# Kernel tuning notes

Measured on AMD Instinct MI355X. Metric: run time of the kernel, lower is better.

The kernel has to match this reference:

```python
import jax, jax.numpy as jnp
import numpy as np

B, N_IN, N_HID, T = 64, 512, 512, 512


def setup_inputs() -> dict:
    key = jax.random.key(0)
    k1, k2, k3, k4, k5 = jax.random.split(key, 5)
    scale = 1.0 / np.sqrt(N_HID).astype(np.float32)
    return {
        "X": jax.random.normal(k1, (B, N_IN, T), dtype=jnp.float32),
        "Wax": jax.random.normal(k2, (N_IN, N_HID), dtype=jnp.float32) * scale,
        "Waa": jax.random.normal(k3, (N_HID, N_HID), dtype=jnp.float32) * scale,
        "bx": jax.random.normal(k4, (N_HID,), dtype=jnp.float32) * scale,
        "ba": jax.random.normal(k5, (N_HID,), dtype=jnp.float32) * scale,
    }


def reference(X, Wax, Waa, bx, ba):
    # X: [B, n_in, T]. a_{t+1} = tanh(x_t @ Wax + bx + a_t @ Waa + ba)
    # Precompute the input projections for all timesteps in one big GEMM:
    # [T, B, n_hid]
    Xt = jnp.transpose(X, (2, 0, 1))  # [T, B, n_in]
    inp_proj = jnp.einsum('tbi,ih->tbh', Xt, Wax) + bx + ba

    def step(a, u):
        a_next = jnp.tanh(u + a @ Waa)
        return a_next, a_next

    a0 = jnp.zeros((X.shape[0], Waa.shape[0]), dtype=X.dtype)
    _, A = jax.lax.scan(step, a0, inp_proj)
    return A  # [T, B, n_hid] == stacked A[1:] of the torch module
```

## Files before the change

kernel.cpp:

```cpp
#include <hip/hip_runtime.h>
#include <math.h>

#define BB   64
#define NIN  512
#define NH   512
#define TT   512

typedef _Float16 half2_t __attribute__((ext_vector_type(2)));

__device__ __forceinline__ unsigned pk16(float x, float y) {
    unsigned lo = (unsigned)__builtin_bit_cast(unsigned short, (_Float16)x);
    unsigned hi = (unsigned)__builtin_bit_cast(unsigned short, (_Float16)y);
    return lo | (hi << 16);
}

__device__ __forceinline__ float dot2u(unsigned w, unsigned a, float acc) {
    return __builtin_amdgcn_fdot2(__builtin_bit_cast(half2_t, w),
                                  __builtin_bit_cast(half2_t, a), acc, false);
}

__device__ __forceinline__ float tanh_fast(float x) {
    float ax = __builtin_fabsf(x);
    float e  = __builtin_amdgcn_exp2f(-2.885390082f * ax);
    float r  = (1.0f - e) * __builtin_amdgcn_rcpf(1.0f + e);
    return __builtin_copysignf(r, x);
}

__global__ __launch_bounds__(256) void inp_proj_fp16(
    const float* __restrict__ X, const float* __restrict__ Wax,
    const float* __restrict__ bx, const float* __restrict__ ba,
    float* __restrict__ out)
{
    __shared__ unsigned Xsp[8][128];
    __shared__ unsigned Wsp[8][128];

    const int b   = blockIdx.z;
    const int t0  = blockIdx.y * 128;
    const int h0  = blockIdx.x * 128;
    const int tid = threadIdx.x;
    const int tx  = tid & 15;
    const int ty  = tid >> 4;
    const int lr  = tid >> 5;
    const int lc  = (tid & 31) * 4;

    const float* Xb = X + (size_t)b * NIN * TT;

    float c[8][8] = {};

    for (int i0 = 0; i0 < NIN; i0 += 16) {
        const int k0 = i0 + 2 * lr, k1 = k0 + 1;
        float4 x0 = *(const float4*)&Xb[(size_t)k0 * TT + t0 + lc];
        float4 x1 = *(const float4*)&Xb[(size_t)k1 * TT + t0 + lc];
        float4 g0 = *(const float4*)&Wax[(size_t)k0 * NH + h0 + lc];
        float4 g1 = *(const float4*)&Wax[(size_t)k1 * NH + h0 + lc];
        uint4 xp, wp;
        xp.x = pk16(x0.x, x1.x); xp.y = pk16(x0.y, x1.y);
        xp.z = pk16(x0.z, x1.z); xp.w = pk16(x0.w, x1.w);
        wp.x = pk16(g0.x, g1.x); wp.y = pk16(g0.y, g1.y);
        wp.z = pk16(g0.z, g1.z); wp.w = pk16(g0.w, g1.w);
        __syncthreads();
        *(uint4*)&Xsp[lr][lc] = xp;
        *(uint4*)&Wsp[lr][lc] = wp;
        __syncthreads();
#pragma unroll
        for (int p = 0; p < 8; ++p) {
            unsigned apk[8], bpk[8];
            *(uint4*)&apk[0] = *(uint4*)&Xsp[p][ty * 8];
            *(uint4*)&apk[4] = *(uint4*)&Xsp[p][ty * 8 + 4];
            *(uint4*)&bpk[0] = *(uint4*)&Wsp[p][tx * 8];
            *(uint4*)&bpk[4] = *(uint4*)&Wsp[p][tx * 8 + 4];
#pragma unroll
            for (int ii = 0; ii < 8; ++ii)
#pragma unroll
                for (int jj = 0; jj < 8; ++jj)
                    c[ii][jj] = dot2u(bpk[jj], apk[ii], c[ii][jj]);
        }
    }

    float bias[8];
#pragma unroll
    for (int j = 0; j < 8; ++j)
        bias[j] = bx[h0 + tx * 8 + j] + ba[h0 + tx * 8 + j];

#pragma unroll
    for (int ii = 0; ii < 8; ++ii) {
        const int t = t0 + ty * 8 + ii;
        float* orow = &out[(size_t)t * (BB * NH) + (size_t)b * NH + h0 + tx * 8];
        float4 v0, v1;
        v0.x = c[ii][0] + bias[0]; v0.y = c[ii][1] + bias[1];
        v0.z = c[ii][2] + bias[2]; v0.w = c[ii][3] + bias[3];
        v1.x = c[ii][4] + bias[4]; v1.y = c[ii][5] + bias[5];
        v1.z = c[ii][6] + bias[6]; v1.w = c[ii][7] + bias[7];
        *(float4*)&orow[0] = v0;
        *(float4*)&orow[4] = v1;
    }
}

#define NRP 52
#define NLP 12
#define PSTRIDE 516

__device__ __forceinline__ unsigned bline(unsigned a, int l) {
    return (unsigned)__builtin_amdgcn_readlane((int)a, l);
}

__global__ __launch_bounds__(512, 2) void rnn_scan_v5(
    const float* __restrict__ Waa, float* __restrict__ out)
{
    __shared__ unsigned wlds[NLP * 4][NH];
    __shared__ unsigned a_lds[2][256];
    __shared__ float    part[4][PSTRIDE];

    const int tid  = threadIdx.x;
    const int b    = blockIdx.x;
    const int cidx = tid & 127;
    const int kq   = tid >> 7;
    const int h4   = cidx * 4;
    const int lane = tid & 63;

    unsigned w0[NRP], w1[NRP], w2[NRP], w3[NRP];
#pragma unroll
    for (int j = 0; j < NRP; ++j) {
        const int k = kq * 128 + 2 * j;
        float4 r0 = *(const float4*)&Waa[(size_t)k       * NH + h4];
        float4 r1 = *(const float4*)&Waa[(size_t)(k + 1) * NH + h4];
        w0[j] = pk16(r0.x, r1.x);
        w1[j] = pk16(r0.y, r1.y);
        w2[j] = pk16(r0.z, r1.z);
        w3[j] = pk16(r0.w, r1.w);
    }
#pragma unroll
    for (int p = 0; p < NLP; ++p) {
        const int k = kq * 128 + 2 * (NRP + p);
        float4 r0 = *(const float4*)&Waa[(size_t)k       * NH + h4];
        float4 r1 = *(const float4*)&Waa[(size_t)(k + 1) * NH + h4];
        wlds[p * 4 + 0][tid] = pk16(r0.x, r1.x);
        wlds[p * 4 + 1][tid] = pk16(r0.y, r1.y);
        wlds[p * 4 + 2][tid] = pk16(r0.z, r1.z);
        wlds[p * 4 + 3][tid] = pk16(r0.w, r1.w);
    }

    if (tid < 256) a_lds[0][tid] = 0u;
    __syncthreads();

    float* ob = out + (size_t)b * NH + tid;
    float u_cur = ob[0];

    for (int t = 0; t < TT; ++t) {
        const int tn = (t + 1 < TT) ? (t + 1) : (TT - 1);
        float u_next = ob[(size_t)tn * (BB * NH)];

        unsigned a_loc = a_lds[t & 1][kq * 64 + lane];

        float acc0 = 0.f, acc1 = 0.f, acc2 = 0.f, acc3 = 0.f;
#pragma unroll
        for (int j = 0; j < NRP; j += 2) {
            unsigned ra = bline(a_loc, j);
            unsigned rb = bline(a_loc, j + 1);
            acc0 = dot2u(w0[j], ra, acc0);
            acc1 = dot2u(w1[j], ra, acc1);
            acc2 = dot2u(w2[j], ra, acc2);
            acc3 = dot2u(w3[j], ra, acc3);
            acc0 = dot2u(w0[j + 1], rb, acc0);
            acc1 = dot2u(w1[j + 1], rb, acc1);
            acc2 = dot2u(w2[j + 1], rb, acc2);
            acc3 = dot2u(w3[j + 1], rb, acc3);
        }
#pragma unroll
        for (int p = 0; p < NLP; ++p) {
            unsigned ra = bline(a_loc, NRP + p);
            unsigned v0 = wlds[p * 4 + 0][tid];
            unsigned v1 = wlds[p * 4 + 1][tid];
            unsigned v2 = wlds[p * 4 + 2][tid];
            unsigned v3 = wlds[p * 4 + 3][tid];
            acc0 = dot2u(v0, ra, acc0);
            acc1 = dot2u(v1, ra, acc1);
            acc2 = dot2u(v2, ra, acc2);
            acc3 = dot2u(v3, ra, acc3);
        }

        float4 pv; pv.x = acc0; pv.y = acc1; pv.z = acc2; pv.w = acc3;
        *(float4*)&part[kq][h4] = pv;
        __builtin_amdgcn_s_waitcnt(0xC07F);
        __builtin_amdgcn_s_barrier();

        float x = u_cur + ((part[0][tid] + part[1][tid]) +
                           (part[2][tid] + part[3][tid]));
        float an = tanh_fast(x);
        ob[(size_t)t * (BB * NH)] = an;
        u_cur = u_next;

        ((unsigned short*)a_lds[(t + 1) & 1])[tid] =
            __builtin_bit_cast(unsigned short, (_Float16)an);
        __builtin_amdgcn_s_waitcnt(0xC07F);
        __builtin_amdgcn_s_barrier();
    }
}

extern "C" void kernel_launch(void* const* d_in, const int* in_sizes, int n_in,
                              void* d_out, int out_size, void* d_ws, size_t ws_size,
                              hipStream_t stream) {
    const float* X   = (const float*)d_in[0];
    const float* Wax = (const float*)d_in[1];
    const float* Waa = (const float*)d_in[2];
    const float* bx  = (const float*)d_in[3];
    const float* ba  = (const float*)d_in[4];
    float* out = (float*)d_out;

    dim3 g1(NH / 128, TT / 128, BB);
    inp_proj_fp16<<<g1, 256, 0, stream>>>(X, Wax, bx, ba, out);
    rnn_scan_v5<<<BB, NH, 0, stream>>>(Waa, out);
}
```

Measured before the change: 1.100 ms.

## Compute input projection GEMM with fp16 MFMA instead of dot2

Rewrites the input-projection kernel to use 16x16x32 fp16 MFMA instructions. Each of four waves computes a 64x64 tile, and the K step widens to 32 with padded LDS tiles. This targets the VALU-bound dot2 GEMM, which is a sizeable part of the total time next to the serial scan. Output stores become scalar per lane, which may coalesce less well than the old float4 stores.

```diff
diff --git a/kernel.cpp b/kernel.cpp
--- a/kernel.cpp
+++ b/kernel.cpp
@@ -7,6 +7,8 @@
 #define TT   512
 
 typedef _Float16 half2_t __attribute__((ext_vector_type(2)));
+typedef _Float16 half8_t __attribute__((ext_vector_type(8)));
+typedef float    f32x4  __attribute__((ext_vector_type(4)));
 
 __device__ __forceinline__ unsigned pk16(float x, float y) {
     unsigned lo = (unsigned)__builtin_bit_cast(unsigned short, (_Float16)x);
@@ -26,73 +28,100 @@
     return __builtin_copysignf(r, x);
 }
 
-__global__ __launch_bounds__(256) void inp_proj_fp16(
+__global__ __launch_bounds__(256) void inp_proj_mfma(
     const float* __restrict__ X, const float* __restrict__ Wax,
     const float* __restrict__ bx, const float* __restrict__ ba,
     float* __restrict__ out)
 {
-    __shared__ unsigned Xsp[8][128];
-    __shared__ unsigned Wsp[8][128];
+    __shared__ unsigned Xsp[16][132];
+    __shared__ unsigned Wsp[16][132];
 
     const int b   = blockIdx.z;
     const int t0  = blockIdx.y * 128;
     const int h0  = blockIdx.x * 128;
     const int tid = threadIdx.x;
-    const int tx  = tid & 15;
-    const int ty  = tid >> 4;
-    const int lr  = tid >> 5;
-    const int lc  = (tid & 31) * 4;
+    const int lane = tid & 63;
+    const int wid  = tid >> 6;
+    const int wm   = wid >> 1;
+    const int wn   = wid & 1;
+    const int q    = lane >> 4;
+    const int r16  = lane & 15;
+
+    const int lr = tid >> 4;
+    const int lc = (tid & 15) * 8;
 
     const float* Xb = X + (size_t)b * NIN * TT;
 
-    float c[8][8] = {};
-
-    for (int i0 = 0; i0 < NIN; i0 += 16) {
+    f32x4 acc[4][4] = {};
+
+    for (int i0 = 0; i0 < NIN; i0 += 32) {
         const int k0 = i0 + 2 * lr, k1 = k0 + 1;
-        float4 x0 = *(const float4*)&Xb[(size_t)k0 * TT + t0 + lc];
-        float4 x1 = *(const float4*)&Xb[(size_t)k1 * TT + t0 + lc];
-        float4 g0 = *(const float4*)&Wax[(size_t)k0 * NH + h0 + lc];
-        float4 g1 = *(const float4*)&Wax[(size_t)k1 * NH + h0 + lc];
-        uint4 xp, wp;
-        xp.x = pk16(x0.x, x1.x); xp.y = pk16(x0.y, x1.y);
-        xp.z = pk16(x0.z, x1.z); xp.w = pk16(x0.w, x1.w);
-        wp.x = pk16(g0.x, g1.x); wp.y = pk16(g0.y, g1.y);
-        wp.z = pk16(g0.z, g1.z); wp.w = pk16(g0.w, g1.w);
+        float4 xa0 = *(const float4*)&Xb[(size_t)k0 * TT + t0 + lc];
+        float4 xa1 = *(const float4*)&Xb[(size_t)k0 * TT + t0 + lc + 4];
+        float4 xb0 = *(const float4*)&Xb[(size_t)k1 * TT + t0 + lc];
+        float4 xb1 = *(const float4*)&Xb[(size_t)k1 * TT + t0 + lc + 4];
+        float4 wa0 = *(const float4*)&Wax[(size_t)k0 * NH + h0 + lc];
+        float4 wa1 = *(const float4*)&Wax[(size_t)k0 * NH + h0 + lc + 4];
+        float4 wb0 = *(const float4*)&Wax[(size_t)k1 * NH + h0 + lc];
+        float4 wb1 = *(const float4*)&Wax[(size_t)k1 * NH + h0 + lc + 4];
+
+        uint4 xp0, xp1, wp0, wp1;
+        xp0.x = pk16(xa0.x, xb0.x); xp0.y = pk16(xa0.y, xb0.y);
+        xp0.z = pk16(xa0.z, xb0.z); xp0.w = pk16(xa0.w, xb0.w);
+        xp1.x = pk16(xa1.x, xb1.x); xp1.y = pk16(xa1.y, xb1.y);
+        xp1.z = pk16(xa1.z, xb1.z); xp1.w = pk16(xa1.w, xb1.w);
+        wp0.x = pk16(wa0.x, wb0.x); wp0.y = pk16(wa0.y, wb0.y);
+        wp0.z = pk16(wa0.z, wb0.z); wp0.w = pk16(wa0.w, wb0.w);
+        wp1.x = pk16(wa1.x, wb1.x); wp1.y = pk16(wa1.y, wb1.y);
+        wp1.z = pk16(wa1.z, wb1.z); wp1.w = pk16(wa1.w, wb1.w);
+
         __syncthreads();
-        *(uint4*)&Xsp[lr][lc] = xp;
-        *(uint4*)&Wsp[lr][lc] = wp;
+        *(uint4*)&Xsp[lr][lc]     = xp0;
+        *(uint4*)&Xsp[lr][lc + 4] = xp1;
+        *(uint4*)&Wsp[lr][lc]     = wp0;
+        *(uint4*)&Wsp[lr][lc + 4] = wp1;
         __syncthreads();
-#pragma unroll
-        for (int p = 0; p < 8; ++p) {
-            unsigned apk[8], bpk[8];
-            *(uint4*)&apk[0] = *(uint4*)&Xsp[p][ty * 8];
-            *(uint4*)&apk[4] = *(uint4*)&Xsp[p][ty * 8 + 4];
-            *(uint4*)&bpk[0] = *(uint4*)&Wsp[p][tx * 8];
-            *(uint4*)&bpk[4] = *(uint4*)&Wsp[p][tx * 8 + 4];
-#pragma unroll
-            for (int ii = 0; ii < 8; ++ii)
-#pragma unroll
-                for (int jj = 0; jj < 8; ++jj)
-                    c[ii][jj] = dot2u(bpk[jj], apk[ii], c[ii][jj]);
-        }
-    }
-
-    float bias[8];
-#pragma unroll
-    for (int j = 0; j < 8; ++j)
-        bias[j] = bx[h0 + tx * 8 + j] + ba[h0 + tx * 8 + j];
-
-#pragma unroll
-    for (int ii = 0; ii < 8; ++ii) {
-        const int t = t0 + ty * 8 + ii;
-        float* orow = &out[(size_t)t * (BB * NH) + (size_t)b * NH + h0 + tx * 8];
-        float4 v0, v1;
-        v0.x = c[ii][0] + bias[0]; v0.y = c[ii][1] + bias[1];
-        v0.z = c[ii][2] + bias[2]; v0.w = c[ii][3] + bias[3];
-        v1.x = c[ii][4] + bias[4]; v1.y = c[ii][5] + bias[5];
-        v1.z = c[ii][6] + bias[6]; v1.w = c[ii][7] + bias[7];
-        *(float4*)&orow[0] = v0;
-        *(float4*)&orow[4] = v1;
+
+        uint4 af[4], bf[4];
+#pragma unroll
+        for (int mt = 0; mt < 4; ++mt) {
+            const int tc = wm * 64 + mt * 16 + r16;
+            af[mt].x = Xsp[4 * q + 0][tc];
+            af[mt].y = Xsp[4 * q + 1][tc];
+            af[mt].z = Xsp[4 * q + 2][tc];
+            af[mt].w = Xsp[4 * q + 3][tc];
+        }
+#pragma unroll
+        for (int nt = 0; nt < 4; ++nt) {
+            const int hc = wn * 64 + nt * 16 + r16;
+            bf[nt].x = Wsp[4 * q + 0][hc];
+            bf[nt].y = Wsp[4 * q + 1][hc];
+            bf[nt].z = Wsp[4 * q + 2][hc];
+            bf[nt].w = Wsp[4 * q + 3][hc];
+        }
+#pragma unroll
+        for (int mt = 0; mt < 4; ++mt)
+#pragma unroll
+            for (int nt = 0; nt < 4; ++nt)
+                acc[mt][nt] = __builtin_amdgcn_mfma_f32_16x16x32_f16(
+                    __builtin_bit_cast(half8_t, af[mt]),
+                    __builtin_bit_cast(half8_t, bf[nt]),
+                    acc[mt][nt], 0, 0, 0);
+    }
+
+#pragma unroll
+    for (int nt = 0; nt < 4; ++nt) {
+        const int h = h0 + wn * 64 + nt * 16 + r16;
+        const float bias = bx[h] + ba[h];
+#pragma unroll
+        for (int mt = 0; mt < 4; ++mt) {
+            const int trow = t0 + wm * 64 + mt * 16 + q * 4;
+#pragma unroll
+            for (int rr = 0; rr < 4; ++rr) {
+                out[(size_t)(trow + rr) * (BB * NH) + (size_t)b * NH + h] =
+                    acc[mt][nt][rr] + bias;
+            }
+        }
     }
 }
 
@@ -208,6 +237,6 @@
     float* out = (float*)d_out;
 
     dim3 g1(NH / 128, TT / 128, BB);
-    inp_proj_fp16<<<g1, 256, 0, stream>>>(X, Wax, bx, ba, out);
+    inp_proj_mfma<<<g1, 256, 0, stream>>>(X, Wax, bx, ba, out);
     rnn_scan_v5<<<BB, NH, 0, stream>>>(Waa, out);
 }
```

Measured after the change: 1.012 ms. -8.0%, faster.
